# Performance work log

Measured on AMD Instinct MI355X. Metric: run time of the kernel, lower is better.

## Reference

```python
import jax, jax.numpy as jnp
import numpy as np

F = 32  # node channels (both convs)


def ecc_conv(x, src, dst, e, fgn_w, fgn_b, root, bias):
    """Edge-conditioned conv: per-edge kernel from edge feats, gather-matmul-scatter."""
    n_nodes = x.shape[0]
    n_edges = e.shape[0]
    f_in = x.shape[1]
    # filter-generating network: (E, S) -> (E, F_in*F_out) -> (E, F_in, F_out)
    kernels = (e @ fgn_w + fgn_b).reshape(n_edges, f_in, F)
    # gather source node feats, per-edge matmul
    messages = jnp.einsum('ef,efo->eo', x[src], kernels)
    # scatter-sum to target nodes
    agg = jax.ops.segment_sum(messages, dst, num_segments=n_nodes)
    return jax.nn.relu(agg + x @ root + bias)


def setup_inputs() -> dict:
    key = jax.random.key(0)
    ks = jax.random.split(key, 12)
    N, E, S = 50000, 200000, 16
    s = 0.05  # small init scale to keep activations bounded through relu
    return {
        'x': jax.random.normal(ks[0], (N, F), jnp.float32),
        'e': jax.random.normal(ks[1], (E, S), jnp.float32),
        'src': jax.random.randint(ks[2], (E,), 0, N, jnp.int32),
        'dst': jax.random.randint(ks[3], (E,), 0, N, jnp.int32),
        'fgn_w1': jax.random.normal(ks[4], (S, F * F), jnp.float32) * s,
        'fgn_b1': jnp.zeros((F * F,), jnp.float32),
        'root1': jax.random.normal(ks[5], (F, F), jnp.float32) * s,
        'bias1': jnp.zeros((F,), jnp.float32),
        'fgn_w2': jax.random.normal(ks[6], (S, F * F), jnp.float32) * s,
        'fgn_b2': jnp.zeros((F * F,), jnp.float32),
        'root2': jax.random.normal(ks[7], (F, F), jnp.float32) * s,
        'bias2': jnp.zeros((F,), jnp.float32),
        'dense_w': jax.random.normal(ks[8], (F, 1), jnp.float32) * s,
        'dense_b': jnp.zeros((1,), jnp.float32),
    }


def reference(x, e, src, dst, fgn_w1, fgn_b1, root1, bias1,
              fgn_w2, fgn_b2, root2, bias2, dense_w, dense_b):
    h = ecc_conv(x, src, dst, e, fgn_w1, fgn_b1, root1, bias1)
    h = ecc_conv(h, src, dst, e, fgn_w2, fgn_b2, root2, bias2)
    pooled = jnp.sum(h, axis=0)          # global sum pool over nodes -> (F,)
    return pooled @ dense_w + dense_b    # (1,)
```

## Files before the change

kernel.cpp:

```cpp
#include <hip/hip_runtime.h>
#include <hip/hip_bf16.h>

#define F 32
#define S 16

typedef short v8s __attribute__((ext_vector_type(8)));
typedef float v4f __attribute__((ext_vector_type(4)));

__device__ __forceinline__ float bf_lo(unsigned u) { return __uint_as_float(u << 16); }
__device__ __forceinline__ float bf_hi(unsigned u) { return __uint_as_float(u & 0xffff0000u); }
__device__ __forceinline__ unsigned short f2bf(float f) {
    __hip_bfloat16 h = __float2bfloat16(f);
    return *(unsigned short*)&h;
}
__device__ __forceinline__ unsigned pack2(float a, float b) {
    __hip_bfloat162 h2 = __float22bfloat162_rn(make_float2(a, b));
    return *(unsigned*)&h2;
}
static inline size_t align256(size_t b) { return (b + 255) & ~(size_t)255; }

__global__ __launch_bounds__(256) void prep_kernel(
    const float* __restrict__ w1, const float* __restrict__ b1, const float* __restrict__ r1,
    const float* __restrict__ w2, const float* __restrict__ b2, const float* __restrict__ r2,
    unsigned short* __restrict__ Wf1, unsigned short* __restrict__ Wf2,
    unsigned short* __restrict__ Rt1, unsigned short* __restrict__ Rt2,
    const int* __restrict__ dst, int* __restrict__ cnt, int E)
{
    const int PER = 34 * 512 + 32 * 32;
    if (blockIdx.x < 144) {
        int tid = blockIdx.x * blockDim.x + threadIdx.x;
        if (tid >= 2 * PER) return;
        const int layer = tid / PER;
        const int rem   = tid % PER;
        const float* w = layer ? w2 : w1;
        const float* b = layer ? b2 : b1;
        const float* r = layer ? r2 : r1;
        if (rem < 34 * 512) {
            const int fi   = rem >> 9;
            const int rr   = rem & 511;
            const int lane = rr >> 3;
            const int j    = rr & 7;
            const int half = fi & 1;
            const int ck   = fi >> 1;
            const int o    = (half << 4) | (lane & 15);
            const int k    = ck * 32 + (lane >> 4) * 8 + j;
            const int s    = k >> 5, f = k & 31;
            const float v  = (s < S) ? w[s * (F * F) + f * F + o] : b[f * F + o];
            (layer ? Wf2 : Wf1)[rem] = f2bf(v);
        } else {
            const int q = rem - 34 * 512;
            const int o = q >> 5, f = q & 31;
            (layer ? Rt2 : Rt1)[o * F + f] = f2bf(r[f * F + o]);
        }
    } else {
        const int e = (blockIdx.x - 144) * blockDim.x + threadIdx.x;
        if (e < E) atomicAdd(&cnt[dst[e]], 1);
    }
}

__global__ __launch_bounds__(256) void scan_partial(
    const int* __restrict__ cnt, int* __restrict__ partial, int N)
{
    const int i = blockIdx.x * 256 + threadIdx.x;
    int v = (i < N) ? cnt[i] : 0;
    #pragma unroll
    for (int off = 32; off > 0; off >>= 1) v += __shfl_down(v, off, 64);
    __shared__ int wsum[4];
    const int wave = threadIdx.x >> 6, lane = threadIdx.x & 63;
    if (lane == 0) wsum[wave] = v;
    __syncthreads();
    if (threadIdx.x == 0)
        partial[blockIdx.x] = wsum[0] + wsum[1] + wsum[2] + wsum[3];
}

__global__ void scan_top(int* __restrict__ partial, int M)
{
    const int t = threadIdx.x;
    int carry = 0;
    for (int base = 0; base < M; base += 64) {
        const int i = base + t;
        const int v0 = (i < M) ? partial[i] : 0;
        int v = v0;
        #pragma unroll
        for (int off = 1; off < 64; off <<= 1) {
            int u = __shfl_up(v, off, 64);
            if (t >= off) v += u;
        }
        if (i < M) partial[i] = carry + (v - v0);
        carry += __shfl(v, 63, 64);
    }
}

__global__ __launch_bounds__(256) void scan_final(
    const int* __restrict__ cnt, const int* __restrict__ partial,
    int* __restrict__ cursor, int* __restrict__ rowptr, int N)
{
    const int i = blockIdx.x * 256 + threadIdx.x;
    const int v0 = (i < N) ? cnt[i] : 0;
    int v = v0;
    const int wave = threadIdx.x >> 6, lane = threadIdx.x & 63;
    #pragma unroll
    for (int off = 1; off < 64; off <<= 1) {
        int u = __shfl_up(v, off, 64);
        if (lane >= off) v += u;
    }
    __shared__ int wsum[4];
    if (lane == 63) wsum[wave] = v;
    __syncthreads();
    int woff = 0;
    for (int ww = 0; ww < 4; ++ww) woff += (ww < wave) ? wsum[ww] : 0;
    if (i < N) {
        const int excl = partial[blockIdx.x] + woff + (v - v0);
        cursor[i] = excl;
        rowptr[i] = excl;
    }
}

__global__ __launch_bounds__(256) void scatter_kernel(
    const int* __restrict__ dst, int* __restrict__ cursor,
    int* __restrict__ perm, int E)
{
    int e = blockIdx.x * blockDim.x + threadIdx.x;
    if (e < E) {
        int p = atomicAdd(&cursor[dst[e]], 1);
        perm[p] = e;
    }
}

__global__ __launch_bounds__(256) void edge_msg(
    const float* __restrict__ xin,
    const float* __restrict__ ef,
    const int* __restrict__ src,
    const unsigned short* __restrict__ Wf,
    unsigned short* __restrict__ msg,
    int E)
{
    __shared__ v8s Wl[34 * 64];
    const int tid  = threadIdx.x;
    const int w    = tid >> 6;
    const int lane = tid & 63;
    const int lid  = lane & 15;
    const int quad = lane >> 4;

    {
        const uint4* s = (const uint4*)Wf;
        uint4* d = (uint4*)Wl;
        #pragma unroll
        for (int i = 0; i < 9; ++i) {
            const int idx = tid + 256 * i;
            if (idx < 2176) d[idx] = s[idx];
        }
    }
    __syncthreads();

    const int nTiles = (E + 15) >> 4;
    const int stride = gridDim.x * 4;
    int tile = blockIdx.x * 4 + w;
    if (tile >= nTiles) return;

    int  slot = tile * 16 + lid;
    bool live = (slot < E);
    int  s0   = live ? slot : 0;
    int  sn   = src[s0];
    const float4* xp = (const float4*)(xin + (size_t)sn * F + quad * 8);
    float4 xv0 = xp[0], xv1 = xp[1];
    const float4* efv = (const float4*)(ef + (size_t)s0 * S);
    float4 c0 = efv[0], c1 = efv[1], c2 = efv[2], c3 = efv[3];

    while (true) {
        const int nextTile = tile + stride;
        float4 nxv0, nxv1, nc0, nc1, nc2, nc3;
        bool nlive = false;
        if (nextTile < nTiles) {
            const int  ns_  = nextTile * 16 + lid;
            nlive = (ns_ < E);
            const int  ns0_ = nlive ? ns_ : 0;
            const int  nsn  = src[ns0_];
            const float4* nxp = (const float4*)(xin + (size_t)nsn * F + quad * 8);
            nxv0 = nxp[0]; nxv1 = nxp[1];
            const float4* nefv = (const float4*)(ef + (size_t)ns0_ * S);
            nc0 = nefv[0]; nc1 = nefv[1]; nc2 = nefv[2]; nc3 = nefv[3];
        }

        const float cs[S] = {c0.x, c0.y, c0.z, c0.w, c1.x, c1.y, c1.z, c1.w,
                             c2.x, c2.y, c2.z, c2.w, c3.x, c3.y, c3.z, c3.w};

        v4f acc0 = {0.f, 0.f, 0.f, 0.f};
        v4f acc1 = {0.f, 0.f, 0.f, 0.f};

        #pragma unroll
        for (int ck = 0; ck < S; ++ck) {
            const float sc = cs[ck];
            union { v8s s8; uint4 u4; } fr;
            fr.u4.x = pack2(sc * xv0.x, sc * xv0.y);
            fr.u4.y = pack2(sc * xv0.z, sc * xv0.w);
            fr.u4.z = pack2(sc * xv1.x, sc * xv1.y);
            fr.u4.w = pack2(sc * xv1.z, sc * xv1.w);
            acc0 = __builtin_amdgcn_mfma_f32_16x16x32_bf16(Wl[(2 * ck) * 64 + lane],     fr.s8, acc0, 0, 0, 0);
            acc1 = __builtin_amdgcn_mfma_f32_16x16x32_bf16(Wl[(2 * ck + 1) * 64 + lane], fr.s8, acc1, 0, 0, 0);
        }
        {
            union { v8s s8; uint4 u4; } fr;
            fr.u4.x = pack2(xv0.x, xv0.y);
            fr.u4.y = pack2(xv0.z, xv0.w);
            fr.u4.z = pack2(xv1.x, xv1.y);
            fr.u4.w = pack2(xv1.z, xv1.w);
            acc0 = __builtin_amdgcn_mfma_f32_16x16x32_bf16(Wl[32 * 64 + lane], fr.s8, acc0, 0, 0, 0);
            acc1 = __builtin_amdgcn_mfma_f32_16x16x32_bf16(Wl[33 * 64 + lane], fr.s8, acc1, 0, 0, 0);
        }

        if (live) {
            unsigned short* mp = msg + (size_t)slot * 32;
            uint2 p0, p1;
            p0.x = pack2(acc0[0], acc0[1]);
            p0.y = pack2(acc0[2], acc0[3]);
            p1.x = pack2(acc1[0], acc1[1]);
            p1.y = pack2(acc1[2], acc1[3]);
            *(uint2*)(mp + quad * 4)      = p0;
            *(uint2*)(mp + 16 + quad * 4) = p1;
        }

        if (nextTile >= nTiles) break;
        tile = nextTile;
        slot = tile * 16 + lid;
        live = nlive;
        xv0 = nxv0; xv1 = nxv1;
        c0 = nc0; c1 = nc1; c2 = nc2; c3 = nc3;
    }
}

__global__ __launch_bounds__(256) void rootsum(
    const float* __restrict__ in,
    const unsigned short* __restrict__ msg,
    const int* __restrict__ rowptr,
    const int* __restrict__ cnt,
    const int* __restrict__ perm,
    const unsigned short* __restrict__ Rt,
    const float* __restrict__ bias,
    float* __restrict__ h,
    int N)
{
    __shared__ float acc[64 * 33];
    __shared__ unsigned short As[64 * F];
    const int tid  = threadIdx.x;
    const int n0   = blockIdx.x * 64;
    const int w    = tid >> 6;
    const int lane = tid & 63;
    const int lid  = lane & 15;
    const int quad = lane >> 4;

    {
        const int nl = tid >> 2;
        const int kq = tid & 3;
        int n = n0 + nl; if (n > N - 1) n = N - 1;
        const float4* xp = (const float4*)(in + (size_t)n * F + kq * 8);
        float4 v0 = xp[0], v1 = xp[1];
        uint4 pk;
        pk.x = pack2(v0.x, v0.y);
        pk.y = pack2(v0.z, v0.w);
        pk.z = pack2(v1.x, v1.y);
        pk.w = pack2(v1.z, v1.w);
        const int slot = ((nl >> 4) * 4 + kq) * 16 + (nl & 15);
        *(uint4*)(As + slot * 8) = pk;
    }

    {
        const int nl = tid >> 2;
        const int oq = tid & 3;
        const int n  = n0 + nl;
        float a[8];
        #pragma unroll
        for (int j = 0; j < 8; ++j) a[j] = 0.f;
        if (n < N) {
            const int k0 = rowptr[n];
            const int k1 = k0 + cnt[n];
            for (int k = k0; k < k1; ++k) {
                const int e = perm[k];
                const uint4 q = *(const uint4*)(msg + (size_t)e * 32 + oq * 8);
                a[0] += bf_lo(q.x); a[1] += bf_hi(q.x);
                a[2] += bf_lo(q.y); a[3] += bf_hi(q.y);
                a[4] += bf_lo(q.z); a[5] += bf_hi(q.z);
                a[6] += bf_lo(q.w); a[7] += bf_hi(q.w);
            }
        }
        float* ap = acc + nl * 33 + oq * 8;
        #pragma unroll
        for (int j = 0; j < 8; ++j) ap[j] = a[j];
    }
    __syncthreads();

    const int jt  = w & 1;
    const int ns0 = (w >> 1) * 2;
    const v8s rf = *(const v8s*)(Rt + (size_t)(jt * 16 + lid) * F + quad * 8);
    const int o0 = jt * 16 + quad * 4;
    const float4 bs = *(const float4*)(bias + o0);

    #pragma unroll
    for (int i = 0; i < 2; ++i) {
        const int ns = ns0 + i;
        const v8s af = *(const v8s*)(As + (((ns * 4 + quad) * 16) + lid) * 8);
        v4f d = {0.f, 0.f, 0.f, 0.f};
        d = __builtin_amdgcn_mfma_f32_16x16x32_bf16(rf, af, d, 0, 0, 0);
        const int n = n0 + ns * 16 + lid;
        if (n < N) {
            const float* ap = acc + (ns * 16 + lid) * 33 + o0;
            float4 hv;
            hv.x = fmaxf(d[0] + ap[0] + bs.x, 0.f);
            hv.y = fmaxf(d[1] + ap[1] + bs.y, 0.f);
            hv.z = fmaxf(d[2] + ap[2] + bs.z, 0.f);
            hv.w = fmaxf(d[3] + ap[3] + bs.w, 0.f);
            *(float4*)(h + (size_t)n * F + o0) = hv;
        }
    }
}

__global__ __launch_bounds__(256) void rootsum_pool(
    const float* __restrict__ in,
    const unsigned short* __restrict__ msg,
    const int* __restrict__ rowptr,
    const int* __restrict__ cnt,
    const int* __restrict__ perm,
    const unsigned short* __restrict__ Rt,
    const float* __restrict__ bias,
    float* __restrict__ bs,
    int N)
{
    __shared__ float acc[64 * 33];
    __shared__ unsigned short As[64 * F];
    __shared__ float poolbuf[4][16];
    const int tid  = threadIdx.x;
    const int n0   = blockIdx.x * 64;
    const int w    = tid >> 6;
    const int lane = tid & 63;
    const int lid  = lane & 15;
    const int quad = lane >> 4;

    {
        const int nl = tid >> 2;
        const int kq = tid & 3;
        int n = n0 + nl; if (n > N - 1) n = N - 1;
        const float4* xp = (const float4*)(in + (size_t)n * F + kq * 8);
        float4 v0 = xp[0], v1 = xp[1];
        uint4 pk;
        pk.x = pack2(v0.x, v0.y);
        pk.y = pack2(v0.z, v0.w);
        pk.z = pack2(v1.x, v1.y);
        pk.w = pack2(v1.z, v1.w);
        const int slot = ((nl >> 4) * 4 + kq) * 16 + (nl & 15);
        *(uint4*)(As + slot * 8) = pk;
    }

    {
        const int nl = tid >> 2;
        const int oq = tid & 3;
        const int n  = n0 + nl;
        float a[8];
        #pragma unroll
        for (int j = 0; j < 8; ++j) a[j] = 0.f;
        if (n < N) {
            const int k0 = rowptr[n];
            const int k1 = k0 + cnt[n];
            for (int k = k0; k < k1; ++k) {
                const int e = perm[k];
                const uint4 q = *(const uint4*)(msg + (size_t)e * 32 + oq * 8);
                a[0] += bf_lo(q.x); a[1] += bf_hi(q.x);
                a[2] += bf_lo(q.y); a[3] += bf_hi(q.y);
                a[4] += bf_lo(q.z); a[5] += bf_hi(q.z);
                a[6] += bf_lo(q.w); a[7] += bf_hi(q.w);
            }
        }
        float* ap = acc + nl * 33 + oq * 8;
        #pragma unroll
        for (int j = 0; j < 8; ++j) ap[j] = a[j];
    }
    __syncthreads();

    const int jt  = w & 1;
    const int ns0 = (w >> 1) * 2;
    const v8s rf = *(const v8s*)(Rt + (size_t)(jt * 16 + lid) * F + quad * 8);
    const int o0 = jt * 16 + quad * 4;
    const float4 bs4 = *(const float4*)(bias + o0);

    float psum[4] = {0.f, 0.f, 0.f, 0.f};

    #pragma unroll
    for (int i = 0; i < 2; ++i) {
        const int ns = ns0 + i;
        const v8s af = *(const v8s*)(As + (((ns * 4 + quad) * 16) + lid) * 8);
        v4f d = {0.f, 0.f, 0.f, 0.f};
        d = __builtin_amdgcn_mfma_f32_16x16x32_bf16(rf, af, d, 0, 0, 0);
        const int n = n0 + ns * 16 + lid;
        if (n < N) {
            const float* ap = acc + (ns * 16 + lid) * 33 + o0;
            psum[0] += fmaxf(d[0] + ap[0] + bs4.x, 0.f);
            psum[1] += fmaxf(d[1] + ap[1] + bs4.y, 0.f);
            psum[2] += fmaxf(d[2] + ap[2] + bs4.z, 0.f);
            psum[3] += fmaxf(d[3] + ap[3] + bs4.w, 0.f);
        }
    }

    #pragma unroll
    for (int m = 1; m < 16; m <<= 1) {
        psum[0] += __shfl_xor(psum[0], m, 64);
        psum[1] += __shfl_xor(psum[1], m, 64);
        psum[2] += __shfl_xor(psum[2], m, 64);
        psum[3] += __shfl_xor(psum[3], m, 64);
    }
    if (lid == 0) {
        #pragma unroll
        for (int j = 0; j < 4; ++j) poolbuf[w][quad * 4 + j] = psum[j];
    }
    __syncthreads();
    if (tid < 32) {
        const int jt2 = tid >> 4, idx = tid & 15;
        bs[(size_t)blockIdx.x * 32 + tid] = poolbuf[jt2][idx] + poolbuf[jt2 + 2][idx];
    }
}

__global__ __launch_bounds__(256) void final_fused(
    const float* __restrict__ bs, int nb,
    const float* __restrict__ dw, const float* __restrict__ db,
    float* __restrict__ out)
{
    const int ch = threadIdx.x & 31, g = threadIdx.x >> 5;
    float s = 0.f;
    for (int b = g; b < nb; b += 8) s += bs[(size_t)b * 32 + ch];
    __shared__ float red[256];
    red[threadIdx.x] = s;
    __syncthreads();
    if (threadIdx.x < 128) red[threadIdx.x] += red[threadIdx.x + 128];
    __syncthreads();
    if (threadIdx.x < 64) red[threadIdx.x] += red[threadIdx.x + 64];
    __syncthreads();
    if (threadIdx.x < 32) red[threadIdx.x] = (red[threadIdx.x] + red[threadIdx.x + 32]) * dw[threadIdx.x];
    __syncthreads();
    if (threadIdx.x == 0) {
        float t = 0.f;
        #pragma unroll
        for (int i = 0; i < 32; ++i) t += red[i];
        out[0] = t + db[0];
    }
}

__global__ __launch_bounds__(256) void pool_kernel(
    const float* __restrict__ h, float* __restrict__ pooled, int N)
{
    const int c = threadIdx.x & (F - 1);
    float p = 0.0f;
    for (int n = blockIdx.x * 8 + (threadIdx.x >> 5); n < N; n += gridDim.x * 8)
        p += h[(size_t)n * F + c];
    __shared__ float red[256];
    red[threadIdx.x] = p;
    __syncthreads();
    for (int off = 128; off >= F; off >>= 1) {
        if (threadIdx.x < off) red[threadIdx.x] += red[threadIdx.x + off];
        __syncthreads();
    }
    if (threadIdx.x < F) atomicAdd(&pooled[threadIdx.x], red[threadIdx.x]);
}

__global__ void final_kernel(
    const float* __restrict__ pooled, const float* __restrict__ dw,
    const float* __restrict__ db, float* __restrict__ out)
{
    const int o = threadIdx.x;
    float v = (o < F) ? pooled[o] * dw[o] : 0.0f;
    #pragma unroll
    for (int off = 32; off > 0; off >>= 1) v += __shfl_down(v, off, 64);
    if (o == 0) out[0] = v + db[0];
}

__global__ __launch_bounds__(256, 2) void ecc_edge_slow(
    const float* __restrict__ x, const float* __restrict__ ef,
    const int* __restrict__ src, const int* __restrict__ dst,
    const float* __restrict__ W, const float* __restrict__ B,
    float* __restrict__ agg, int E)
{
    const int tid = blockIdx.x * blockDim.x + threadIdx.x;
    const bool live = (tid < E);
    const int e = live ? tid : (E - 1);
    const int sn = src[e], dn = dst[e];
    float xr[F];
    const float4* xp = (const float4*)(x + (size_t)sn * F);
    #pragma unroll
    for (int i = 0; i < F / 4; ++i) {
        float4 v = xp[i];
        xr[4*i+0] = v.x; xr[4*i+1] = v.y; xr[4*i+2] = v.z; xr[4*i+3] = v.w;
    }
    float acc[F];
    #pragma unroll
    for (int o = 0; o < F; ++o) acc[o] = 0.0f;
    const float* erow = ef + (size_t)e * S;
    for (int s = 0; s < S; ++s) {
        const float es = erow[s];
        const float* Ws = W + s * (F * F);
        #pragma unroll
        for (int f = 0; f < F; ++f) {
            const float z = es * xr[f];
            #pragma unroll
            for (int o = 0; o < F; ++o) acc[o] = fmaf(z, Ws[f * F + o], acc[o]);
        }
    }
    #pragma unroll
    for (int f = 0; f < F; ++f) {
        const float xf = xr[f];
        #pragma unroll
        for (int o = 0; o < F; ++o) acc[o] = fmaf(xf, B[f * F + o], acc[o]);
    }
    if (live) {
        float* ap = agg + (size_t)dn * F;
        #pragma unroll
        for (int o = 0; o < F; ++o) atomicAdd(ap + o, acc[o]);
    }
}

__global__ __launch_bounds__(256) void ecc_node_slow(
    const float* __restrict__ xin, const float* __restrict__ root,
    const float* __restrict__ bias, float* __restrict__ h, int N)
{
    int t = blockIdx.x * blockDim.x + threadIdx.x;
    if (t >= N * F) return;
    const int n = t >> 5, o = t & (F - 1);
    const float* xrow = xin + (size_t)n * F;
    float v = h[t] + bias[o];
    #pragma unroll
    for (int f = 0; f < F; ++f) v = fmaf(xrow[f], root[f * F + o], v);
    h[t] = fmaxf(v, 0.0f);
}

extern "C" void kernel_launch(void* const* d_in, const int* in_sizes, int n_in,
                              void* d_out, int out_size, void* d_ws, size_t ws_size,
                              hipStream_t stream) {
    const float* x      = (const float*)d_in[0];
    const float* efeat  = (const float*)d_in[1];
    const int*   src    = (const int*)d_in[2];
    const int*   dst    = (const int*)d_in[3];
    const float* fgn_w1 = (const float*)d_in[4];
    const float* fgn_b1 = (const float*)d_in[5];
    const float* root1  = (const float*)d_in[6];
    const float* bias1  = (const float*)d_in[7];
    const float* fgn_w2 = (const float*)d_in[8];
    const float* fgn_b2 = (const float*)d_in[9];
    const float* root2  = (const float*)d_in[10];
    const float* bias2  = (const float*)d_in[11];
    const float* dense_w = (const float*)d_in[12];
    const float* dense_b = (const float*)d_in[13];

    const int N = in_sizes[0] / F;
    const int E = in_sizes[2];

    const int gridP    = (N + 255) / 256;
    const int rsBlocks = (N + 63) / 64;

    const size_t pooledB = 256;
    const size_t cntB    = align256((size_t)N * 4);
    const size_t rowB    = align256((size_t)N * 4);
    const size_t curB    = align256((size_t)N * 4);
    const size_t partB   = align256((size_t)gridP * 4);
    const size_t permB   = align256((size_t)E * 4);
    const size_t efsB    = align256((size_t)E * S * 4);
    const size_t srcsB   = align256((size_t)E * 4);
    const size_t msgB    = align256((size_t)E * 32 * 2);
    const size_t hB      = (size_t)N * F * 4;
    const size_t wfB     = align256((size_t)34 * 512 * 2);
    const size_t rtB     = align256((size_t)32 * 32 * 2);

    const size_t offCnt  = pooledB;
    const size_t offRow  = offCnt + cntB;
    const size_t offCur  = offRow + rowB;
    const size_t offPart = offCur + curB;
    const size_t offPerm = offPart + partB;
    const size_t offEfs  = offPerm + permB;
    const size_t offSrcs = offEfs + efsB;
    const size_t offMsg  = offSrcs + srcsB;
    const size_t offH1   = offMsg + msgB;
    const size_t offH2   = offH1 + hB;
    const size_t offW1   = offH2 + hB;
    const size_t offW2   = offW1 + wfB;
    const size_t offR1   = offW2 + wfB;
    const size_t offR2   = offR1 + rtB;
    const size_t need    = offR2 + rtB;

    const int eB         = (E + 255) / 256;
    const int nodeBlocks = (N * F + 255) / 256;

    if (ws_size >= need) {
        int* cnt     = (int*)((char*)d_ws + offCnt);
        int* rowptr  = (int*)((char*)d_ws + offRow);
        int* cursor  = (int*)((char*)d_ws + offCur);
        int* partial = (int*)((char*)d_ws + offPart);
        int* perm    = (int*)((char*)d_ws + offPerm);
        unsigned short* msg = (unsigned short*)((char*)d_ws + offMsg);
        float* h1    = (float*)((char*)d_ws + offH1);
        float* bsum  = (float*)((char*)d_ws + offH2);
        unsigned short* Wf1 = (unsigned short*)((char*)d_ws + offW1);
        unsigned short* Wf2 = (unsigned short*)((char*)d_ws + offW2);
        unsigned short* Rt1 = (unsigned short*)((char*)d_ws + offR1);
        unsigned short* Rt2 = (unsigned short*)((char*)d_ws + offR2);

        hipMemsetAsync(d_ws, 0, pooledB + cntB, stream);

        prep_kernel<<<144 + eB, 256, 0, stream>>>(
            fgn_w1, fgn_b1, root1, fgn_w2, fgn_b2, root2,
            Wf1, Wf2, Rt1, Rt2, dst, cnt, E);

        scan_partial  <<<gridP, 256, 0, stream>>>(cnt, partial, N);
        scan_top      <<<1, 64, 0, stream>>>(partial, gridP);
        scan_final    <<<gridP, 256, 0, stream>>>(cnt, partial, cursor, rowptr, N);
        scatter_kernel<<<eB, 256, 0, stream>>>(dst, cursor, perm, E);

        const int nTiles = (E + 15) / 16;
        int edgeBlocks = (nTiles + 3) / 4;
        if (edgeBlocks > 1024) edgeBlocks = 1024;

        edge_msg<<<edgeBlocks, 256, 0, stream>>>(x, efeat, src, Wf1, msg, E);
        rootsum <<<rsBlocks, 256, 0, stream>>>(x, msg, rowptr, cnt, perm, Rt1, bias1, h1, N);

        edge_msg    <<<edgeBlocks, 256, 0, stream>>>(h1, efeat, src, Wf2, msg, E);
        rootsum_pool<<<rsBlocks, 256, 0, stream>>>(h1, msg, rowptr, cnt, perm, Rt2, bias2, bsum, N);

        final_fused<<<1, 256, 0, stream>>>(bsum, rsBlocks, dense_w, dense_b, (float*)d_out);
    } else {
        float* agg1   = (float*)d_ws;
        float* agg2   = agg1 + (size_t)N * F;
        float* pooled = agg2 + (size_t)N * F;
        hipMemsetAsync(d_ws, 0, (2 * (size_t)N * F + F) * sizeof(float), stream);
        ecc_edge_slow<<<eB, 256, 0, stream>>>(x, efeat, src, dst, fgn_w1, fgn_b1, agg1, E);
        ecc_node_slow<<<nodeBlocks, 256, 0, stream>>>(x, root1, bias1, agg1, N);
        ecc_edge_slow<<<eB, 256, 0, stream>>>(agg1, efeat, src, dst, fgn_w2, fgn_b2, agg2, E);
        ecc_node_slow<<<nodeBlocks, 256, 0, stream>>>(agg1, root2, bias2, agg2, N);
        pool_kernel <<<512, 256, 0, stream>>>(agg2, pooled, N);
        final_kernel<<<1, 64, 0, stream>>>(pooled, dense_w, dense_b, (float*)d_out);
    }
}
```

Baseline: 207.8 us.

## Fuse CSR build and weight prep into one cooperative grid-synced kernel

Replaces the memset, prep kernel, three-stage scan and scatter kernel with a single cooperative kernel. It zeroes the counts, repacks the weights, counts destinations, scans and fills the permutation, with grid.sync between phases. The aim is to remove several kernel launches and their inter-kernel gaps. In exchange it adds five grid-wide barriers and needs a grid small enough for cooperative launch; the old path is kept as a fallback when the grid is too large.

```diff
diff --git a/kernel.cpp b/kernel.cpp
--- a/kernel.cpp
+++ b/kernel.cpp
@@ -1,5 +1,8 @@
 #include <hip/hip_runtime.h>
 #include <hip/hip_bf16.h>
+#include <hip/hip_cooperative_groups.h>
+
+namespace cg = cooperative_groups;
 
 #define F 32
 #define S 16
@@ -18,6 +21,109 @@
     return *(unsigned*)&h2;
 }
 static inline size_t align256(size_t b) { return (b + 255) & ~(size_t)255; }
+
+__global__ __launch_bounds__(256) void csr_coop(
+    const float* __restrict__ w1, const float* __restrict__ b1, const float* __restrict__ r1,
+    const float* __restrict__ w2, const float* __restrict__ b2, const float* __restrict__ r2,
+    unsigned short* __restrict__ Wf1, unsigned short* __restrict__ Wf2,
+    unsigned short* __restrict__ Rt1, unsigned short* __restrict__ Rt2,
+    const int* __restrict__ dst, int* __restrict__ cnt,
+    int* __restrict__ partial, int* __restrict__ cursor,
+    int* __restrict__ rowptr, int* __restrict__ perm,
+    int N, int E)
+{
+    cg::grid_group grid = cg::this_grid();
+    const int tid  = threadIdx.x;
+    const int gid  = blockIdx.x * 256 + tid;
+    const int GT   = gridDim.x * 256;
+    const int wave = tid >> 6, lane = tid & 63;
+    __shared__ int ws[4];
+
+    for (int i = gid; i < N; i += GT) cnt[i] = 0;
+    {
+        const int PER = 34 * 512 + 32 * 32;
+        for (int t = gid; t < 2 * PER; t += GT) {
+            const int layer = t / PER;
+            const int rem   = t % PER;
+            const float* w = layer ? w2 : w1;
+            const float* b = layer ? b2 : b1;
+            const float* r = layer ? r2 : r1;
+            if (rem < 34 * 512) {
+                const int fi   = rem >> 9;
+                const int rr   = rem & 511;
+                const int ln   = rr >> 3;
+                const int j    = rr & 7;
+                const int half = fi & 1;
+                const int ck   = fi >> 1;
+                const int o    = (half << 4) | (ln & 15);
+                const int k    = ck * 32 + (ln >> 4) * 8 + j;
+                const int s    = k >> 5, f = k & 31;
+                const float v  = (s < S) ? w[s * (F * F) + f * F + o] : b[f * F + o];
+                (layer ? Wf2 : Wf1)[rem] = f2bf(v);
+            } else {
+                const int q = rem - 34 * 512;
+                const int o = q >> 5, f = q & 31;
+                (layer ? Rt2 : Rt1)[o * F + f] = f2bf(r[f * F + o]);
+            }
+        }
+    }
+    grid.sync();
+
+    for (int e = gid; e < E; e += GT) atomicAdd(&cnt[dst[e]], 1);
+    grid.sync();
+
+    const int i   = gid;
+    const int c0  = (i < N) ? cnt[i] : 0;
+    int cv = c0;
+    #pragma unroll
+    for (int off = 1; off < 64; off <<= 1) {
+        int u = __shfl_up(cv, off, 64);
+        if (lane >= off) cv += u;
+    }
+    if (lane == 63) ws[wave] = cv;
+    __syncthreads();
+    int woff = 0;
+    for (int ww = 0; ww < 4; ++ww) woff += (ww < wave) ? ws[ww] : 0;
+    const int my_excl = woff + (cv - c0);
+    if (tid == 0) partial[blockIdx.x] = ws[0] + ws[1] + ws[2] + ws[3];
+    grid.sync();
+
+    if (blockIdx.x == 0) {
+        const int M = gridDim.x;
+        int carry = 0;
+        for (int base = 0; base < M; base += 256) {
+            const int ii = base + tid;
+            const int v0 = (ii < M) ? partial[ii] : 0;
+            int v = v0;
+            #pragma unroll
+            for (int off = 1; off < 64; off <<= 1) {
+                int u = __shfl_up(v, off, 64);
+                if (lane >= off) v += u;
+            }
+            if (lane == 63) ws[wave] = v;
+            __syncthreads();
+            int wo = 0;
+            for (int ww = 0; ww < 4; ++ww) wo += (ww < wave) ? ws[ww] : 0;
+            const int tot = ws[0] + ws[1] + ws[2] + ws[3];
+            if (ii < M) partial[ii] = carry + wo + (v - v0);
+            carry += tot;
+            __syncthreads();
+        }
+    }
+    grid.sync();
+
+    if (i < N) {
+        const int excl = partial[blockIdx.x] + my_excl;
+        rowptr[i] = excl;
+        cursor[i] = excl;
+    }
+    grid.sync();
+
+    for (int e = gid; e < E; e += GT) {
+        int p = atomicAdd(&cursor[dst[e]], 1);
+        perm[p] = e;
+    }
+}
 
 __global__ __launch_bounds__(256) void prep_kernel(
     const float* __restrict__ w1, const float* __restrict__ b1, const float* __restrict__ r1,
@@ -598,16 +704,30 @@
         unsigned short* Rt1 = (unsigned short*)((char*)d_ws + offR1);
         unsigned short* Rt2 = (unsigned short*)((char*)d_ws + offR2);
 
-        hipMemsetAsync(d_ws, 0, pooledB + cntB, stream);
-
-        prep_kernel<<<144 + eB, 256, 0, stream>>>(
-            fgn_w1, fgn_b1, root1, fgn_w2, fgn_b2, root2,
-            Wf1, Wf2, Rt1, Rt2, dst, cnt, E);
-
-        scan_partial  <<<gridP, 256, 0, stream>>>(cnt, partial, N);
-        scan_top      <<<1, 64, 0, stream>>>(partial, gridP);
-        scan_final    <<<gridP, 256, 0, stream>>>(cnt, partial, cursor, rowptr, N);
-        scatter_kernel<<<eB, 256, 0, stream>>>(dst, cursor, perm, E);
+        if (gridP <= 1024) {
+            const float *a0 = fgn_w1, *a1 = fgn_b1, *a2 = root1;
+            const float *a3 = fgn_w2, *a4 = fgn_b2, *a5 = root2;
+            unsigned short *a6 = Wf1, *a7 = Wf2, *a8 = Rt1, *a9 = Rt2;
+            const int *a10 = dst;
+            int *a11 = cnt, *a12 = partial, *a13 = cursor, *a14 = rowptr, *a15 = perm;
+            int a16 = N, a17 = E;
+            void* kargs[] = {
+                (void*)&a0, (void*)&a1, (void*)&a2, (void*)&a3, (void*)&a4, (void*)&a5,
+                (void*)&a6, (void*)&a7, (void*)&a8, (void*)&a9, (void*)&a10,
+                (void*)&a11, (void*)&a12, (void*)&a13, (void*)&a14, (void*)&a15,
+                (void*)&a16, (void*)&a17 };
+            hipLaunchCooperativeKernel((const void*)csr_coop,
+                                       dim3(gridP), dim3(256), kargs, 0, stream);
+        } else {
+            hipMemsetAsync((char*)d_ws + offCnt, 0, cntB, stream);
+            prep_kernel<<<144 + eB, 256, 0, stream>>>(
+                fgn_w1, fgn_b1, root1, fgn_w2, fgn_b2, root2,
+                Wf1, Wf2, Rt1, Rt2, dst, cnt, E);
+            scan_partial  <<<gridP, 256, 0, stream>>>(cnt, partial, N);
+            scan_top      <<<1, 64, 0, stream>>>(partial, gridP);
+            scan_final    <<<gridP, 256, 0, stream>>>(cnt, partial, cursor, rowptr, N);
+            scatter_kernel<<<eB, 256, 0, stream>>>(dst, cursor, perm, E);
+        }
 
         const int nTiles = (E + 15) / 16;
         int edgeBlocks = (nTiles + 3) / 4;
```

Result: slower. 327.3 us (+57.5%).
